# Optimization experiments

Measured on AMD Instinct MI355X. Metric: run time of the kernel, lower is better.

## Reference

```python
import jax, jax.numpy as jnp
import numpy as np

SIGMA = 0.2
BN_EPS = 1e-5


def setup_inputs() -> dict:
    key = jax.random.key(0)
    k1, k2, k3, k4 = jax.random.split(key, 4)
    B, N, K = 8, 16384, 64
    normals = jax.random.normal(k1, (B, 3, N), dtype=jnp.float32)
    # normalize to unit normals (faithful to what the module consumes in practice)
    normals = normals / jnp.linalg.norm(normals, axis=1, keepdims=True)
    neighbor_idx = jax.random.randint(k2, (B, N, 3), 0, N, dtype=jnp.int64)
    weight_alpha = jax.random.uniform(k3, (1, K, 4), dtype=jnp.float32) * np.pi
    weight_beta = jax.random.uniform(k4, (1, K, 4), dtype=jnp.float32) * (2 * np.pi)
    bn_gamma = jnp.ones((K,), dtype=jnp.float32)
    bn_beta = jnp.zeros((K,), dtype=jnp.float32)
    return {
        "normals": normals,
        "neighbor_idx": neighbor_idx,
        "weight_alpha": weight_alpha,
        "weight_beta": weight_beta,
        "bn_gamma": bn_gamma,
        "bn_beta": bn_beta,
    }


def reference(normals, neighbor_idx, weight_alpha, weight_beta, bn_gamma, bn_beta):
    # normals: (B, 3, N); neighbor_idx: (B, N, 3)
    # kernel directions on unit sphere: W[c, k, m], c in xyz, m in 4 points per kernel
    W = jnp.concatenate(
        [
            jnp.sin(weight_alpha) * jnp.cos(weight_beta),
            jnp.sin(weight_alpha) * jnp.sin(weight_beta),
            jnp.cos(weight_alpha),
        ],
        axis=0,
    )  # (3, K, 4)

    # gather neighbor normals: nbr[b, c, i, j] = normals[b, c, neighbor_idx[b, i, j]]
    nbr = jax.vmap(lambda nm, idx: nm[:, idx])(normals, neighbor_idx)  # (B, 3, N, 3)
    F = jnp.concatenate([normals[:, :, :, None], nbr], axis=3)  # (B, 3, N, 4) face points p

    # squared distances via ||f||^2 + ||w||^2 - 2 f.w  (avoids 6D broadcast of torch code)
    dots = jnp.einsum("bcnp,ckm->bknpm", F, W)  # (B, K, N, 4, 4)
    F2 = jnp.sum(F * F, axis=1)[:, None, :, :, None]  # (B, 1, N, 4, 1)
    W2 = jnp.sum(W * W, axis=0)[None, :, None, None, :]  # (1, K, 1, 1, 4)
    dist = F2 + W2 - 2.0 * dots  # (B, K, N, 4, 4)

    inv = -1.0 / (2.0 * SIGMA * SIGMA)
    feat = jnp.sum(jnp.exp(dist * inv), axis=(3, 4)) / 16.0  # (B, K, N)

    # BatchNorm1d (training mode, biased variance over batch+spatial dims) + ReLU
    mean = jnp.mean(feat, axis=(0, 2), keepdims=True)
    var = jnp.var(feat, axis=(0, 2), keepdims=True)
    xhat = (feat - mean) * jax.lax.rsqrt(var + BN_EPS)
    out = bn_gamma[None, :, None] * xhat + bn_beta[None, :, None]
    return jax.nn.relu(out)
```

## Files before the change

kernel.cpp:

```cpp
#include <hip/hip_runtime.h>

#define BB 8
#define NN 16384
#define KK 64
#define NPG 512

#if __has_builtin(__builtin_amdgcn_exp2f)
#define EXP2(x) __builtin_amdgcn_exp2f(x)
#else
#define EXP2(x) exp2f(x)
#endif

#define LOG2E 1.44269504088896340736f
#define CW (25.0f * LOG2E)
#define CE (-12.5f * LOG2E)

__global__ __launch_bounds__(256) void fkc_prep(
    const float* __restrict__ walpha,
    const float* __restrict__ wbeta,
    float* __restrict__ wx,
    float* __restrict__ wy,
    float* __restrict__ wz)
{
    const int t = threadIdx.x;
    float a = walpha[t];
    float b = wbeta[t];
    float sa = __sinf(a);
    wx[t] = CW * sa * __cosf(b);
    wy[t] = CW * sa * __sinf(b);
    wz[t] = CW * __cosf(a);
}

__global__ __launch_bounds__(256, 8) void fkc_main(
    const float* __restrict__ normals,
    const int*   __restrict__ nidx,
    const float* __restrict__ wx,
    const float* __restrict__ wy,
    const float* __restrict__ wz,
    float* __restrict__ out,
    float* __restrict__ psum,
    float* __restrict__ pss)
{
    __shared__ float reds[16][4];
    __shared__ float redss[16][4];

    const int tid = threadIdx.x;
    const int pg = blockIdx.x >> 2;
    const int k0 = (blockIdx.x & 3) * 16;
    const int gid = pg * 256 + tid;
    const int b = gid >> 14;
    const int n = gid & (NN - 1);
    const float* nb = normals + b * 3 * NN;

    float fx[4], fy[4], fz[4], e2[4];
    fx[0] = nb[n];
    fy[0] = nb[NN + n];
    fz[0] = nb[2 * NN + n];
    const int ibase = (b * NN + n) * 3;
#pragma unroll
    for (int j = 0; j < 3; ++j) {
        int id = nidx[ibase + j];
        fx[j + 1] = nb[id];
        fy[j + 1] = nb[NN + id];
        fz[j + 1] = nb[2 * NN + id];
    }
#pragma unroll
    for (int p = 0; p < 4; ++p) {
        float n2 = fmaf(fx[p], fx[p], fmaf(fy[p], fy[p], fz[p] * fz[p]));
        e2[p] = CE * (n2 + 1.0f);
    }

    const int lane = tid & 63;
    const int wv = tid >> 6;
    float* orow = out + (b * KK + k0) * NN + n;

#pragma unroll
    for (int kk = 0; kk < 16; ++kk) {
        float acc = 0.0f;
#pragma unroll
        for (int m = 0; m < 4; ++m) {
            const int wi = ((k0 + kk) << 2) + m;
            float wxv = wx[wi], wyv = wy[wi], wzv = wz[wi];
#pragma unroll
            for (int p = 0; p < 4; ++p) {
                float arg = fmaf(fz[p], wzv,
                            fmaf(fy[p], wyv,
                            fmaf(fx[p], wxv, e2[p])));
                acc += EXP2(arg);
            }
        }
        orow[kk * NN] = acc;

        float s = acc, ss = acc * acc;
#pragma unroll
        for (int off = 1; off < 64; off <<= 1) {
            s  += __shfl_xor(s,  off, 64);
            ss += __shfl_xor(ss, off, 64);
        }
        if (lane == 0) { reds[kk][wv] = s; redss[kk][wv] = ss; }
    }
    __syncthreads();

    if (tid < 16) {
        psum[(k0 + tid) * NPG + pg] =
            reds[tid][0] + reds[tid][1] + reds[tid][2] + reds[tid][3];
    } else if (tid < 32) {
        int kk = tid - 16;
        pss[(k0 + kk) * NPG + pg] =
            redss[kk][0] + redss[kk][1] + redss[kk][2] + redss[kk][3];
    }
}

__global__ __launch_bounds__(256) void fkc_stats(
    const float* __restrict__ psum,
    const float* __restrict__ pss,
    const float* __restrict__ gamma,
    const float* __restrict__ beta,
    float* __restrict__ fin)
{
    __shared__ float sw[4], ssw[4];
    const int tid = threadIdx.x;
    const int k = blockIdx.x;

    float s  = psum[k * NPG + tid] + psum[k * NPG + 256 + tid];
    float ss = pss[k * NPG + tid]  + pss[k * NPG + 256 + tid];
#pragma unroll
    for (int off = 1; off < 64; off <<= 1) {
        s  += __shfl_xor(s,  off, 64);
        ss += __shfl_xor(ss, off, 64);
    }
    const int wv = tid >> 6;
    if ((tid & 63) == 0) { sw[wv] = s; ssw[wv] = ss; }
    __syncthreads();
    if (tid == 0) {
        float st  = sw[0] + sw[1] + sw[2] + sw[3];
        float sst = ssw[0] + ssw[1] + ssw[2] + ssw[3];
        const float invM = 1.0f / (float)(BB * NN);
        float mean = st * invM;
        float var = fmaf(-mean, mean, sst * invM);
        float sc = gamma[k] * rsqrtf(var + 1e-5f);
        fin[k] = sc;
        fin[KK + k] = fmaf(-mean, sc, beta[k]);
    }
}

__global__ __launch_bounds__(256) void fkc_apply(
    float4* __restrict__ out4,
    const float* __restrict__ fin)
{
    const int i = blockIdx.x * 256 + threadIdx.x;
    const int k = (i >> 12) & (KK - 1);
    const float sc = fin[k];
    const float sh = fin[KK + k];
    float4 v = out4[i];
    v.x = fmaxf(fmaf(v.x, sc, sh), 0.0f);
    v.y = fmaxf(fmaf(v.y, sc, sh), 0.0f);
    v.z = fmaxf(fmaf(v.z, sc, sh), 0.0f);
    v.w = fmaxf(fmaf(v.w, sc, sh), 0.0f);
    out4[i] = v;
}

extern "C" void kernel_launch(void* const* d_in, const int* in_sizes, int n_in,
                              void* d_out, int out_size, void* d_ws, size_t ws_size,
                              hipStream_t stream) {
    const float* normals = (const float*)d_in[0];
    const int*   nidx    = (const int*)d_in[1];
    const float* walpha  = (const float*)d_in[2];
    const float* wbeta   = (const float*)d_in[3];
    const float* gamma   = (const float*)d_in[4];
    const float* beta    = (const float*)d_in[5];
    float* out = (float*)d_out;
    float* ws = (float*)d_ws;

    float* psum = ws;
    float* pss  = ws + KK * NPG;
    float* fin  = ws + 2 * KK * NPG;
    float* wxb  = ws + 2 * KK * NPG + 128;
    float* wyb  = wxb + 256;
    float* wzb  = wyb + 256;

    fkc_prep<<<1, 256, 0, stream>>>(walpha, wbeta, wxb, wyb, wzb);
    fkc_main<<<2048, 256, 0, stream>>>(normals, nidx, wxb, wyb, wzb,
                                       out, psum, pss);
    fkc_stats<<<KK, 256, 0, stream>>>(psum, pss, gamma, beta, fin);
    fkc_apply<<<8192, 256, 0, stream>>>((float4*)out, fin);
}
```

Baseline: 118.1 us.

## Fuse feature, batch-norm stats and apply into one cooperative kernel

Replaces the main, stats and apply kernels with a single cooperative-groups kernel. Each thread keeps 32 features in registers, and grid-wide syncs separate the partial-sum, stats and normalize phases. This removes the unnormalized output write plus the read-modify-write pass over the 32 MB output, and cuts launch overhead. In exchange it needs all 1024 blocks resident, with the launch bound lowered to 5 blocks per CU, and pays for two grid barriers. If the cooperative launch fails it falls back to the old three-kernel path.

```diff
diff --git a/kernel.cpp b/kernel.cpp
--- a/kernel.cpp
+++ b/kernel.cpp
@@ -1,4 +1,7 @@
 #include <hip/hip_runtime.h>
+#include <hip/hip_cooperative_groups.h>
+
+namespace cg = cooperative_groups;
 
 #define BB 8
 #define NN 16384
@@ -16,11 +19,8 @@
 #define CE (-12.5f * LOG2E)
 
 __global__ __launch_bounds__(256) void fkc_prep(
-    const float* __restrict__ walpha,
-    const float* __restrict__ wbeta,
-    float* __restrict__ wx,
-    float* __restrict__ wy,
-    float* __restrict__ wz)
+    const float* __restrict__ walpha, const float* __restrict__ wbeta,
+    float* __restrict__ wx, float* __restrict__ wy, float* __restrict__ wz)
 {
     const int t = threadIdx.x;
     float a = walpha[t];
@@ -31,15 +31,134 @@
     wz[t] = CW * __cosf(a);
 }
 
-__global__ __launch_bounds__(256, 8) void fkc_main(
+__global__ __launch_bounds__(256, 5) void fkc_fused(
     const float* __restrict__ normals,
     const int*   __restrict__ nidx,
-    const float* __restrict__ wx,
-    const float* __restrict__ wy,
+    const float* __restrict__ wx, const float* __restrict__ wy,
     const float* __restrict__ wz,
+    const float* __restrict__ gamma, const float* __restrict__ beta,
     float* __restrict__ out,
     float* __restrict__ psum,
-    float* __restrict__ pss)
+    float* __restrict__ pss,
+    float* __restrict__ fin)
+{
+    cg::grid_group grid = cg::this_grid();
+
+    __shared__ float reds[32][4];
+    __shared__ float redss[32][4];
+    __shared__ float fsc[KK], fsh[KK];
+
+    const int tid = threadIdx.x;
+    const int bid = blockIdx.x;
+    const int pg = bid >> 1;
+    const int k0 = (bid & 1) * 32;
+    const int gid = pg * 256 + tid;
+    const int b = gid >> 14;
+    const int n = gid & (NN - 1);
+    const float* nb = normals + b * 3 * NN;
+
+    float fx[4], fy[4], fz[4], e2[4];
+    fx[0] = nb[n];
+    fy[0] = nb[NN + n];
+    fz[0] = nb[2 * NN + n];
+    const int ibase = (b * NN + n) * 3;
+#pragma unroll
+    for (int j = 0; j < 3; ++j) {
+        int id = nidx[ibase + j];
+        fx[j + 1] = nb[id];
+        fy[j + 1] = nb[NN + id];
+        fz[j + 1] = nb[2 * NN + id];
+    }
+#pragma unroll
+    for (int p = 0; p < 4; ++p) {
+        float n2 = fmaf(fx[p], fx[p], fmaf(fy[p], fy[p], fz[p] * fz[p]));
+        e2[p] = CE * (n2 + 1.0f);
+    }
+
+    const int lane = tid & 63;
+    const int wv = tid >> 6;
+    float feats[32];
+#pragma unroll 4
+    for (int kk = 0; kk < 32; ++kk) {
+        float acc = 0.0f;
+#pragma unroll
+        for (int m = 0; m < 4; ++m) {
+            const int wi = ((k0 + kk) << 2) + m;
+            float wxv = wx[wi], wyv = wy[wi], wzv = wz[wi];
+#pragma unroll
+            for (int p = 0; p < 4; ++p) {
+                float arg = fmaf(fz[p], wzv,
+                            fmaf(fy[p], wyv,
+                            fmaf(fx[p], wxv, e2[p])));
+                acc += EXP2(arg);
+            }
+        }
+        feats[kk] = acc;
+        float s = acc, ss = acc * acc;
+#pragma unroll
+        for (int off = 1; off < 64; off <<= 1) {
+            s  += __shfl_xor(s,  off, 64);
+            ss += __shfl_xor(ss, off, 64);
+        }
+        if (lane == 0) { reds[kk][wv] = s; redss[kk][wv] = ss; }
+    }
+    __syncthreads();
+    if (tid < 32) {
+        psum[(k0 + tid) * NPG + pg] =
+            reds[tid][0] + reds[tid][1] + reds[tid][2] + reds[tid][3];
+    } else if (tid < 64) {
+        int kk = tid - 32;
+        pss[(k0 + kk) * NPG + pg] =
+            redss[kk][0] + redss[kk][1] + redss[kk][2] + redss[kk][3];
+    }
+
+    grid.sync();
+
+    if (bid < KK) {
+        const int k = bid;
+        float s  = psum[k * NPG + tid] + psum[k * NPG + 256 + tid];
+        float ss = pss[k * NPG + tid]  + pss[k * NPG + 256 + tid];
+#pragma unroll
+        for (int off = 1; off < 64; off <<= 1) {
+            s  += __shfl_xor(s,  off, 64);
+            ss += __shfl_xor(ss, off, 64);
+        }
+        if (lane == 0) { reds[0][wv] = s; redss[0][wv] = ss; }
+        __syncthreads();
+        if (tid == 0) {
+            float st  = reds[0][0] + reds[0][1] + reds[0][2] + reds[0][3];
+            float sst = redss[0][0] + redss[0][1] + redss[0][2] + redss[0][3];
+            const float invM = 1.0f / (float)(BB * NN);
+            float mean = st * invM;
+            float var = fmaf(-mean, mean, sst * invM);
+            float sc = gamma[k] * rsqrtf(var + 1e-5f);
+            fin[k] = sc;
+            fin[KK + k] = fmaf(-mean, sc, beta[k]);
+        }
+    }
+
+    grid.sync();
+
+    if (tid < 2 * KK) {
+        float v = fin[tid];
+        if (tid < KK) fsc[tid] = v; else fsh[tid - KK] = v;
+    }
+    __syncthreads();
+
+    float* orow = out + (b * KK + k0) * NN + n;
+#pragma unroll 4
+    for (int kk = 0; kk < 32; ++kk) {
+        float sc = fsc[k0 + kk];
+        float sh = fsh[k0 + kk];
+        orow[kk * NN] = fmaxf(fmaf(feats[kk], sc, sh), 0.0f);
+    }
+}
+
+__global__ __launch_bounds__(256, 8) void fkc_main(
+    const float* __restrict__ normals, const int* __restrict__ nidx,
+    const float* __restrict__ wx, const float* __restrict__ wy,
+    const float* __restrict__ wz,
+    float* __restrict__ out, float* __restrict__ psum, float* __restrict__ pss)
 {
     __shared__ float reds[16][4];
     __shared__ float redss[16][4];
@@ -90,7 +209,6 @@
             }
         }
         orow[kk * NN] = acc;
-
         float s = acc, ss = acc * acc;
 #pragma unroll
         for (int off = 1; off < 64; off <<= 1) {
@@ -112,10 +230,8 @@
 }
 
 __global__ __launch_bounds__(256) void fkc_stats(
-    const float* __restrict__ psum,
-    const float* __restrict__ pss,
-    const float* __restrict__ gamma,
-    const float* __restrict__ beta,
+    const float* __restrict__ psum, const float* __restrict__ pss,
+    const float* __restrict__ gamma, const float* __restrict__ beta,
     float* __restrict__ fin)
 {
     __shared__ float sw[4], ssw[4];
@@ -145,8 +261,7 @@
 }
 
 __global__ __launch_bounds__(256) void fkc_apply(
-    float4* __restrict__ out4,
-    const float* __restrict__ fin)
+    float4* __restrict__ out4, const float* __restrict__ fin)
 {
     const int i = blockIdx.x * 256 + threadIdx.x;
     const int k = (i >> 12) & (KK - 1);
@@ -180,8 +295,17 @@
     float* wzb  = wyb + 256;
 
     fkc_prep<<<1, 256, 0, stream>>>(walpha, wbeta, wxb, wyb, wzb);
-    fkc_main<<<2048, 256, 0, stream>>>(normals, nidx, wxb, wyb, wzb,
-                                       out, psum, pss);
-    fkc_stats<<<KK, 256, 0, stream>>>(psum, pss, gamma, beta, fin);
-    fkc_apply<<<8192, 256, 0, stream>>>((float4*)out, fin);
-}
+
+    void* args[] = { &normals, &nidx, &wxb, &wyb, &wzb, &gamma, &beta,
+                     &out, &psum, &pss, &fin };
+    hipError_t err = hipLaunchCooperativeKernel((const void*)fkc_fused,
+                                                dim3(1024), dim3(256),
+                                                args, 0, stream);
+    if (err != hipSuccess) {
+        (void)hipGetLastError();
+        fkc_main<<<2048, 256, 0, stream>>>(normals, nidx, wxb, wyb, wzb,
+                                           out, psum, pss);
+        fkc_stats<<<KK, 256, 0, stream>>>(psum, pss, gamma, beta, fin);
+        fkc_apply<<<8192, 256, 0, stream>>>((float4*)out, fin);
+    }
+}
```

New measurement: 314.1 us. 2.66x slower.

## Move BN statistics out of main kernel into separate reduce pass over output

Applied to the files above, without the earlier changes.

The main kernel no longer does per-k wavefront shuffles, shared-memory reductions or block-wide syncs. It only computes and stores features. A new reduce kernel rereads the full 32 MB output to compute per-channel partial sums, and the apply kernel now finalises mean/variance inline, which removes the stats kernel. This trades the shuffle/sync overhead in the compute-bound main kernel for an extra full read of the output tensor.

```diff
diff --git a/kernel.cpp b/kernel.cpp
--- a/kernel.cpp
+++ b/kernel.cpp
@@ -3,7 +3,6 @@
 #define BB 8
 #define NN 16384
 #define KK 64
-#define NPG 512
 
 #if __has_builtin(__builtin_amdgcn_exp2f)
 #define EXP2(x) __builtin_amdgcn_exp2f(x)
@@ -16,11 +15,8 @@
 #define CE (-12.5f * LOG2E)
 
 __global__ __launch_bounds__(256) void fkc_prep(
-    const float* __restrict__ walpha,
-    const float* __restrict__ wbeta,
-    float* __restrict__ wx,
-    float* __restrict__ wy,
-    float* __restrict__ wz)
+    const float* __restrict__ walpha, const float* __restrict__ wbeta,
+    float* __restrict__ wx, float* __restrict__ wy, float* __restrict__ wz)
 {
     const int t = threadIdx.x;
     float a = walpha[t];
@@ -34,16 +30,10 @@
 __global__ __launch_bounds__(256, 8) void fkc_main(
     const float* __restrict__ normals,
     const int*   __restrict__ nidx,
-    const float* __restrict__ wx,
-    const float* __restrict__ wy,
+    const float* __restrict__ wx, const float* __restrict__ wy,
     const float* __restrict__ wz,
-    float* __restrict__ out,
-    float* __restrict__ psum,
-    float* __restrict__ pss)
+    float* __restrict__ out)
 {
-    __shared__ float reds[16][4];
-    __shared__ float redss[16][4];
-
     const int tid = threadIdx.x;
     const int pg = blockIdx.x >> 2;
     const int k0 = (blockIdx.x & 3) * 16;
@@ -70,10 +60,7 @@
         e2[p] = CE * (n2 + 1.0f);
     }
 
-    const int lane = tid & 63;
-    const int wv = tid >> 6;
     float* orow = out + (b * KK + k0) * NN + n;
-
 #pragma unroll
     for (int kk = 0; kk < 16; ++kk) {
         float acc = 0.0f;
@@ -90,40 +77,31 @@
             }
         }
         orow[kk * NN] = acc;
-
-        float s = acc, ss = acc * acc;
-#pragma unroll
-        for (int off = 1; off < 64; off <<= 1) {
-            s  += __shfl_xor(s,  off, 64);
-            ss += __shfl_xor(ss, off, 64);
-        }
-        if (lane == 0) { reds[kk][wv] = s; redss[kk][wv] = ss; }
-    }
-    __syncthreads();
-
-    if (tid < 16) {
-        psum[(k0 + tid) * NPG + pg] =
-            reds[tid][0] + reds[tid][1] + reds[tid][2] + reds[tid][3];
-    } else if (tid < 32) {
-        int kk = tid - 16;
-        pss[(k0 + kk) * NPG + pg] =
-            redss[kk][0] + redss[kk][1] + redss[kk][2] + redss[kk][3];
     }
 }
 
-__global__ __launch_bounds__(256) void fkc_stats(
-    const float* __restrict__ psum,
-    const float* __restrict__ pss,
-    const float* __restrict__ gamma,
-    const float* __restrict__ beta,
-    float* __restrict__ fin)
+__global__ __launch_bounds__(256) void fkc_reduce(
+    const float4* __restrict__ out4,
+    float* __restrict__ psum,
+    float* __restrict__ pss)
 {
     __shared__ float sw[4], ssw[4];
     const int tid = threadIdx.x;
-    const int k = blockIdx.x;
+    const int k = blockIdx.x >> 2;
+    const int c = blockIdx.x & 3;
 
-    float s  = psum[k * NPG + tid] + psum[k * NPG + 256 + tid];
-    float ss = pss[k * NPG + tid]  + pss[k * NPG + 256 + tid];
+    float s = 0.0f, ss = 0.0f;
+#pragma unroll
+    for (int r = 0; r < 2; ++r) {
+        const int b = 2 * c + r;
+        const int base4 = (b * KK + k) * (NN / 4);
+#pragma unroll
+        for (int j = 0; j < 16; ++j) {
+            float4 v = out4[base4 + tid + j * 256];
+            s += (v.x + v.y) + (v.z + v.w);
+            ss += fmaf(v.x, v.x, fmaf(v.y, v.y, fmaf(v.z, v.z, v.w * v.w)));
+        }
+    }
 #pragma unroll
     for (int off = 1; off < 64; off <<= 1) {
         s  += __shfl_xor(s,  off, 64);
@@ -133,25 +111,31 @@
     if ((tid & 63) == 0) { sw[wv] = s; ssw[wv] = ss; }
     __syncthreads();
     if (tid == 0) {
-        float st  = sw[0] + sw[1] + sw[2] + sw[3];
-        float sst = ssw[0] + ssw[1] + ssw[2] + ssw[3];
-        const float invM = 1.0f / (float)(BB * NN);
-        float mean = st * invM;
-        float var = fmaf(-mean, mean, sst * invM);
-        float sc = gamma[k] * rsqrtf(var + 1e-5f);
-        fin[k] = sc;
-        fin[KK + k] = fmaf(-mean, sc, beta[k]);
+        psum[k * 4 + c] = sw[0] + sw[1] + sw[2] + sw[3];
+        pss[k * 4 + c]  = ssw[0] + ssw[1] + ssw[2] + ssw[3];
     }
 }
 
 __global__ __launch_bounds__(256) void fkc_apply(
     float4* __restrict__ out4,
-    const float* __restrict__ fin)
+    const float* __restrict__ psum,
+    const float* __restrict__ pss,
+    const float* __restrict__ gamma,
+    const float* __restrict__ beta)
 {
     const int i = blockIdx.x * 256 + threadIdx.x;
     const int k = (i >> 12) & (KK - 1);
-    const float sc = fin[k];
-    const float sh = fin[KK + k];
+
+    float st  = (psum[k * 4 + 0] + psum[k * 4 + 1]) +
+                (psum[k * 4 + 2] + psum[k * 4 + 3]);
+    float sst = (pss[k * 4 + 0] + pss[k * 4 + 1]) +
+                (pss[k * 4 + 2] + pss[k * 4 + 3]);
+    const float invM = 1.0f / (float)(BB * NN);
+    float mean = st * invM;
+    float var = fmaf(-mean, mean, sst * invM);
+    float sc = gamma[k] * rsqrtf(var + 1e-5f);
+    float sh = fmaf(-mean, sc, beta[k]);
+
     float4 v = out4[i];
     v.x = fmaxf(fmaf(v.x, sc, sh), 0.0f);
     v.y = fmaxf(fmaf(v.y, sc, sh), 0.0f);
@@ -173,15 +157,13 @@
     float* ws = (float*)d_ws;
 
     float* psum = ws;
-    float* pss  = ws + KK * NPG;
-    float* fin  = ws + 2 * KK * NPG;
-    float* wxb  = ws + 2 * KK * NPG + 128;
-    float* wyb  = wxb + 256;
-    float* wzb  = wyb + 256;
+    float* pss  = ws + 256;
+    float* wxb  = ws + 512;
+    float* wyb  = ws + 768;
+    float* wzb  = ws + 1024;
 
     fkc_prep<<<1, 256, 0, stream>>>(walpha, wbeta, wxb, wyb, wzb);
-    fkc_main<<<2048, 256, 0, stream>>>(normals, nidx, wxb, wyb, wzb,
-                                       out, psum, pss);
-    fkc_stats<<<KK, 256, 0, stream>>>(psum, pss, gamma, beta, fin);
-    fkc_apply<<<8192, 256, 0, stream>>>((float4*)out, fin);
+    fkc_main<<<2048, 256, 0, stream>>>(normals, nidx, wxb, wyb, wzb, out);
+    fkc_reduce<<<256, 256, 0, stream>>>((const float4*)out, psum, pss);
+    fkc_apply<<<8192, 256, 0, stream>>>((float4*)out, psum, pss, gamma, beta);
 }
```

New measurement: 116.6 us. No clear change (-1.2%).
